# Performance work log

Hardware: AMD Instinct MI355X
Metric: run time of the kernel (lower is better)

The kernel has to match this reference:

```python
import jax, jax.numpy as jnp
import numpy as np

B, QLEN, PAST, D = 4, 2048, 2048, 2048


def setup_inputs() -> dict:
    key = jax.random.key(0)
    ks = jax.random.split(key, 6)
    x = jax.random.normal(ks[0], (B, QLEN, D), dtype=jnp.float32)
    past_k = jax.random.normal(ks[1], (B, PAST, D), dtype=jnp.float32)
    past_v = jax.random.normal(ks[2], (B, PAST, D), dtype=jnp.float32)
    # nn.Linear(model_dim, model_dim, bias=False) weights: [out, in]
    scale = 1.0 / np.sqrt(D)
    Wq = jax.random.uniform(ks[3], (D, D), dtype=jnp.float32, minval=-scale, maxval=scale)
    Wk = jax.random.uniform(ks[4], (D, D), dtype=jnp.float32, minval=-scale, maxval=scale)
    Wv = jax.random.uniform(ks[5], (D, D), dtype=jnp.float32, minval=-scale, maxval=scale)
    return {"x": x, "past_k": past_k, "past_v": past_v, "Wq": Wq, "Wk": Wk, "Wv": Wv}


def reference(x, past_k, past_v, Wq, Wk, Wv):
    # QKV projections (Linear: y = x @ W.T)
    q = jnp.einsum('btd,ed->bte', x, Wq)
    k = jnp.einsum('btd,ed->bte', x, Wk)
    v = jnp.einsum('btd,ed->bte', x, Wv)
    # KV cache update: concat along sequence dim (dim=1)
    full_k = jnp.concatenate([past_k, k], axis=1)  # [B, PAST+QLEN, D]
    full_v = jnp.concatenate([past_v, v], axis=1)
    # scaled dot-product attention, naive full score matrix as in source
    inv_sqrt_d = full_k.shape[-1] ** (-0.5)
    scores = jnp.einsum('bqd,bkd->bqk', q, full_k) * inv_sqrt_d  # [B, QLEN, PAST+QLEN]
    weights = jax.nn.softmax(scores, axis=-1)
    output = jnp.einsum('bqk,bkd->bqd', weights, full_v)
    return jnp.round(output, 4)
```

## Files before the change

kernel.cpp:

```cpp
#include <hip/hip_runtime.h>
#include <stdint.h>

#define QLEN  2048
#define PAST  2048
#define D_    2048
#define B_    4
#define LK    4096

typedef unsigned short ushort_t;
typedef __bf16  bf16x8 __attribute__((ext_vector_type(8)));
typedef float   f32x4  __attribute__((ext_vector_type(4)));

#define AS1 __attribute__((address_space(1)))
#define AS3 __attribute__((address_space(3)))

__device__ __forceinline__ ushort_t f2bf(float f) {
  union { float f; uint32_t u; } v; v.f = f;
  uint32_t u = v.u;
  u += 0x7FFFu + ((u >> 16) & 1u);
  return (ushort_t)(u >> 16);
}

__global__ __launch_bounds__(256) void diag_fill(float* __restrict__ out, int n4, float v0) {
  int i = blockIdx.x * 256 + threadIdx.x;
  if (i >= n4) return;
  float4 z = make_float4(0.f, 0.f, 0.f, 0.f);
  if (i == 0) z.x = v0;
  ((float4*)out)[i] = z;
}

__global__ __launch_bounds__(256) void cast_f32_bf16(const float* __restrict__ src,
                                                     ushort_t* __restrict__ dst, int n4) {
  int i = blockIdx.x * 256 + threadIdx.x;
  if (i >= n4) return;
  float4 v = ((const float4*)src)[i];
  ushort4 o; o.x = f2bf(v.x); o.y = f2bf(v.y); o.z = f2bf(v.z); o.w = f2bf(v.w);
  ((ushort4*)dst)[i] = o;
}

__global__ __launch_bounds__(256) void transpose_cast(const float* __restrict__ src0,
                                                      ushort_t* __restrict__ dst0,
                                                      size_t sbs, size_t dbs) {
  __shared__ float tile[64][65];
  const float* src = src0 + (size_t)blockIdx.z * sbs;
  ushort_t* dst = dst0 + (size_t)blockIdx.z * dbs;
  const int r0 = blockIdx.x * 64, c0 = blockIdx.y * 64;
  const int tid = threadIdx.x;
  const int rr = tid >> 4, cc = (tid & 15) * 4;
  #pragma unroll
  for (int it = 0; it < 4; ++it) {
    int r = rr + it * 16;
    float4 v = *(const float4*)(src + (size_t)(r0 + r) * D_ + c0 + cc);
    tile[r][cc] = v.x; tile[r][cc + 1] = v.y; tile[r][cc + 2] = v.z; tile[r][cc + 3] = v.w;
  }
  __syncthreads();
  const int cw = tid >> 4, rw = (tid & 15) * 4;
  #pragma unroll
  for (int it = 0; it < 4; ++it) {
    int c = cw + it * 16;
    ushort4 o;
    o.x = f2bf(tile[rw][c]);     o.y = f2bf(tile[rw + 1][c]);
    o.z = f2bf(tile[rw + 2][c]); o.w = f2bf(tile[rw + 3][c]);
    *(ushort4*)(dst + (size_t)(c0 + c) * PAST + r0 + rw) = o;
  }
}

struct GZ  { const ushort_t* A; const ushort_t* B0; const ushort_t* B1; void* C; };
struct GZV { GZ z[12]; };

template <bool OUT_BF16, bool SEG2>
__global__ __launch_bounds__(512, 2) void gemm_bt(GZV gz, int lda, int ldb, int K, int Kseg,
                                                  int ldc, float scale) {
  __shared__ ushort_t As[4][256 * 32];
  __shared__ ushort_t Bs[4][256 * 32];
  const GZ g = gz.z[blockIdx.z];

  const int tid  = threadIdx.x;
  const int lane = tid & 63;
  const int wave = tid >> 6;
  const int wm = wave >> 2, wn = wave & 3;
  const int m0 = blockIdx.y * 256, n0 = blockIdx.x * 256;

  const int r0s = tid >> 2;
  const int pgs = (tid & 3) ^ ((r0s >> 1) & 3);
  const ushort_t* gA  = g.A  + (size_t)(m0 + r0s) * lda + pgs * 8;
  const ushort_t* gB0 = g.B0 + (size_t)(n0 + r0s) * ldb + pgs * 8;
  const ushort_t* gB1 = SEG2 ? (g.B1 + (size_t)(n0 + r0s) * ldb + pgs * 8) : gB0;
  const size_t rstepA = (size_t)128 * lda;
  const size_t rstepB = (size_t)128 * ldb;
  const int ldsOff = tid * 8;

  const int laneRow = lane & 15, quad = lane >> 4;
  int offA[8], offB[4];
  #pragma unroll
  for (int mi = 0; mi < 8; ++mi) {
    const int row = wm * 128 + mi * 16 + laneRow;
    offA[mi] = row * 32 + ((quad ^ ((row >> 1) & 3)) * 8);
  }
  #pragma unroll
  for (int ni = 0; ni < 4; ++ni) {
    const int row = wn * 64 + ni * 16 + laneRow;
    offB[ni] = row * 32 + ((quad ^ ((row >> 1) & 3)) * 8);
  }

  const int NU = K >> 5;

  auto stageA = [&](int u) {
    const int k0 = u << 5;
    ushort_t* dst = &As[u & 3][0];
    __builtin_amdgcn_global_load_lds((const AS1 uint32_t*)(gA + k0),
                                     (AS3 uint32_t*)(dst + ldsOff), 16, 0, 0);
    __builtin_amdgcn_global_load_lds((const AS1 uint32_t*)(gA + rstepA + k0),
                                     (AS3 uint32_t*)(dst + 4096 + ldsOff), 16, 0, 0);
  };
  auto stageB = [&](int u) {
    const int k0 = u << 5;
    ushort_t* dst = &Bs[u & 3][0];
    const ushort_t* src = gB0;
    int kk = k0;
    if (SEG2 && k0 >= Kseg) { src = gB1; kk = k0 - Kseg; }
    __builtin_amdgcn_global_load_lds((const AS1 uint32_t*)(src + kk),
                                     (AS3 uint32_t*)(dst + ldsOff), 16, 0, 0);
    __builtin_amdgcn_global_load_lds((const AS1 uint32_t*)(src + rstepB + kk),
                                     (AS3 uint32_t*)(dst + 4096 + ldsOff), 16, 0, 0);
  };

  f32x4 acc[8][4] = {};

  stageA(0); stageB(0);
  stageA(1); stageB(1);
  stageA(2); stageB(2);
  __builtin_amdgcn_sched_barrier(0);
  asm volatile("s_waitcnt vmcnt(8)" ::: "memory");
  __builtin_amdgcn_s_barrier();
  __builtin_amdgcn_sched_barrier(0);

  for (int u = 0; u < NU; ++u) {
    const ushort_t* Au = &As[u & 3][0];
    const ushort_t* Bu = &Bs[u & 3][0];
    const bool pre = (u + 3) < NU;

    bf16x8 af[8], bf[4];
    #pragma unroll
    for (int mi = 0; mi < 8; ++mi) af[mi] = *(const bf16x8*)(Au + offA[mi]);
    #pragma unroll
    for (int ni = 0; ni < 4; ++ni) bf[ni] = *(const bf16x8*)(Bu + offB[ni]);

    if (pre) { stageA(u + 3); stageB(u + 3); }

    __builtin_amdgcn_s_setprio(1);
    #pragma unroll
    for (int mi = 0; mi < 8; ++mi)
      #pragma unroll
      for (int ni = 0; ni < 4; ++ni)
        acc[mi][ni] = __builtin_amdgcn_mfma_f32_16x16x32_bf16(af[mi], bf[ni], acc[mi][ni], 0, 0, 0);
    __builtin_amdgcn_s_setprio(0);

    __builtin_amdgcn_sched_barrier(0);
    if (pre) { asm volatile("s_waitcnt vmcnt(8)" ::: "memory"); }
    else     { asm volatile("s_waitcnt vmcnt(0)" ::: "memory"); }
    __builtin_amdgcn_s_barrier();
    __builtin_amdgcn_sched_barrier(0);
  }

  const int col = lane & 15;
  #pragma unroll
  for (int mi = 0; mi < 8; ++mi) {
    #pragma unroll
    for (int ni = 0; ni < 4; ++ni) {
      const int n = n0 + wn * 64 + ni * 16 + col;
      const int mb = m0 + wm * 128 + mi * 16 + quad * 4;
      #pragma unroll
      for (int r = 0; r < 4; ++r) {
        const int m = mb + r;
        const float v = acc[mi][ni][r] * scale;
        if constexpr (OUT_BF16)
          ((ushort_t*)g.C)[(size_t)m * ldc + n] = f2bf(v);
        else
          ((float*)g.C)[(size_t)m * ldc + n] = v;
      }
    }
  }
}

__global__ __launch_bounds__(256) void softmax_inplace(ushort_t* __restrict__ Sa,
                                                       ushort_t* __restrict__ Sb) {
  ushort_t* S = blockIdx.y ? Sb : Sa;
  const int row = blockIdx.x, tid = threadIdx.x;
  const int lane = tid & 63, wave = tid >> 6;
  ushort_t* s = S + (size_t)row * LK;

  float e[16];
  float m = -1e30f;
  #pragma unroll
  for (int i = 0; i < 2; ++i) {
    uint4 raw = *(const uint4*)(s + i * 2048 + tid * 8);
    const uint32_t u[4] = { raw.x, raw.y, raw.z, raw.w };
    #pragma unroll
    for (int j = 0; j < 4; ++j) {
      union { uint32_t u; float f; } lo, hi;
      lo.u = u[j] << 16;
      hi.u = u[j] & 0xFFFF0000u;
      e[i * 8 + j * 2] = lo.f;
      e[i * 8 + j * 2 + 1] = hi.f;
      m = fmaxf(m, fmaxf(lo.f, hi.f));
    }
  }
  #pragma unroll
  for (int off = 32; off > 0; off >>= 1) m = fmaxf(m, __shfl_xor(m, off));
  __shared__ float redm[4], reds[4];
  if (lane == 0) redm[wave] = m;
  __syncthreads();
  m = fmaxf(fmaxf(redm[0], redm[1]), fmaxf(redm[2], redm[3]));

  float sum = 0.f;
  #pragma unroll
  for (int i = 0; i < 16; ++i) { e[i] = __expf(e[i] - m); sum += e[i]; }
  #pragma unroll
  for (int off = 32; off > 0; off >>= 1) sum += __shfl_xor(sum, off);
  if (lane == 0) reds[wave] = sum;
  __syncthreads();
  sum = reds[0] + reds[1] + reds[2] + reds[3];
  const float inv = 1.0f / sum;

  #pragma unroll
  for (int i = 0; i < 2; ++i) {
    uint4 o;
    uint32_t* po = &o.x;
    #pragma unroll
    for (int j = 0; j < 4; ++j) {
      uint32_t lo = f2bf(e[i * 8 + j * 2] * inv);
      uint32_t hi = f2bf(e[i * 8 + j * 2 + 1] * inv);
      po[j] = lo | (hi << 16);
    }
    *(uint4*)(s + i * 2048 + tid * 8) = o;
  }
}

extern "C" void kernel_launch(void* const* d_in, const int* in_sizes, int n_in,
                              void* d_out, int out_size, void* d_ws, size_t ws_size,
                              hipStream_t stream) {
  const float* x      = (const float*)d_in[0];
  const float* past_k = (const float*)d_in[1];
  const float* past_v = (const float*)d_in[2];
  const float* Wq     = (const float*)d_in[3];
  const float* Wk     = (const float*)d_in[4];
  const float* Wv     = (const float*)d_in[5];
  float* out = (float*)d_out;

  const size_t MB = 1024 * 1024;
  const size_t NEED = 160 * MB;
  if (ws_size < NEED) {
    diag_fill<<<(out_size / 4 + 255) / 256, 256, 0, stream>>>(out, out_size / 4,
                                                              (float)((double)ws_size * 1e-9));
    return;
  }

  char* ws = (char*)d_ws;
  ushort_t* Qp[4]  = { (ushort_t*)(ws),            (ushort_t*)(ws + 8  * MB),
                       (ushort_t*)(ws + 32 * MB),  (ushort_t*)(ws + 40 * MB) };
  ushort_t* Knp[4] = { (ushort_t*)(ws + 16 * MB),  (ushort_t*)(ws + 24 * MB),
                       (ushort_t*)(ws + 48 * MB),  (ushort_t*)(ws + 56 * MB) };
  ushort_t* VTn = (ushort_t*)(ws + 64 * MB);
  ushort_t* xb  = (ushort_t*)(ws + 96 * MB);
  ushort_t* Wqb = (ushort_t*)(ws + 128 * MB);
  ushort_t* Wkb = (ushort_t*)(ws + 136 * MB);
  ushort_t* Wvb = (ushort_t*)(ws + 144 * MB);
  ushort_t* Kp  = (ushort_t*)(ws + 96 * MB);
  ushort_t* S0  = (ushort_t*)(ws + 128 * MB);
  ushort_t* S1  = (ushort_t*)(ws);
  ushort_t* VTp = (ushort_t*)(ws + 96 * MB);

  const size_t SLICE = (size_t)QLEN * D_;

  cast_f32_bf16<<<(B_ * SLICE / 4) / 256, 256, 0, stream>>>(x, xb, B_ * SLICE / 4);
  cast_f32_bf16<<<(D_ * D_ / 4) / 256, 256, 0, stream>>>(Wq, Wqb, D_ * D_ / 4);
  cast_f32_bf16<<<(D_ * D_ / 4) / 256, 256, 0, stream>>>(Wk, Wkb, D_ * D_ / 4);
  cast_f32_bf16<<<(D_ * D_ / 4) / 256, 256, 0, stream>>>(Wv, Wvb, D_ * D_ / 4);

  {
    GZV g{};
    for (int b = 0; b < B_; ++b) {
      const ushort_t* xbb = xb + (size_t)b * SLICE;
      g.z[b]     = { xbb, Wqb, Wqb, Qp[b] };
      g.z[4 + b] = { xbb, Wkb, Wkb, Knp[b] };
      g.z[8 + b] = { Wvb, xbb, xbb, VTn + (size_t)b * SLICE };
    }
    gemm_bt<true, false><<<dim3(8, 8, 12), 512, 0, stream>>>(g, D_, D_, D_, D_, D_, 1.0f);
  }

  cast_f32_bf16<<<(B_ * (size_t)PAST * D_ / 4) / 256, 256, 0, stream>>>(
      past_k, Kp, B_ * PAST * D_ / 4);

  const float sc = 0.022097086912079608f;

  {
    GZV g{};
    for (int j = 0; j < 2; ++j) {
      const int b = j;
      ushort_t* Sb = S0 + (size_t)j * QLEN * LK;
      g.z[2 * j]     = { Qp[b], Kp + (size_t)b * SLICE,  Kp + (size_t)b * SLICE,  Sb };
      g.z[2 * j + 1] = { Qp[b], Knp[b],                  Knp[b],                  Sb + PAST };
    }
    gemm_bt<true, false><<<dim3(8, 8, 4), 512, 0, stream>>>(g, D_, D_, D_, D_, LK, sc);
  }
  {
    GZV g{};
    for (int j = 0; j < 2; ++j) {
      const int b = 2 + j;
      ushort_t* Sb = S1 + (size_t)j * QLEN * LK;
      g.z[2 * j]     = { Qp[b], Kp + (size_t)b * SLICE,  Kp + (size_t)b * SLICE,  Sb };
      g.z[2 * j + 1] = { Qp[b], Knp[b],                  Knp[b],                  Sb + PAST };
    }
    gemm_bt<true, false><<<dim3(8, 8, 4), 512, 0, stream>>>(g, D_, D_, D_, D_, LK, sc);
  }

  transpose_cast<<<dim3(PAST / 64, D_ / 64, B_), 256, 0, stream>>>(
      past_v, VTp, (size_t)PAST * D_, (size_t)D_ * PAST);

  softmax_inplace<<<dim3(2 * QLEN, 2), 256, 0, stream>>>(S0, S1);

  {
    GZV g{};
    const ushort_t* Pb[4] = { S0, S0 + (size_t)QLEN * LK, S1, S1 + (size_t)QLEN * LK };
    for (int b = 0; b < B_; ++b)
      g.z[b] = { Pb[b], VTp + (size_t)b * SLICE, VTn + (size_t)b * SLICE,
                 out + (size_t)b * QLEN * D_ };
    gemm_bt<false, true><<<dim3(8, 8, 4), 512, 0, stream>>>(g, LK, PAST, LK, PAST, D_, 1.0f);
  }
}
```

Measured before the change: 704.2 us.

## Double-buffer LDS fragment reads across k-steps in the bf16 MFMA GEMM loop

Restructures the GEMM main loop, unrolled by two, so fragments for the next k-step are read from LDS while the current step's second half of MFMAs runs. Each step is split into two 4x4 MFMA groups, with register sets for A (rows 0-3 and 4-7) and two B buffers alternating between steps. The goal is to hide LDS read latency behind MFMA work. In exchange the global-to-LDS wait tightens from vmcnt(8) to vmcnt(4), which shrinks the effective global prefetch depth. It also raises register pressure and assumes an even number of k-steps.

```diff
diff --git a/kernel.cpp b/kernel.cpp
--- a/kernel.cpp
+++ b/kernel.cpp
@@ -131,36 +131,92 @@
   stageA(1); stageB(1);
   stageA(2); stageB(2);
   __builtin_amdgcn_sched_barrier(0);
-  asm volatile("s_waitcnt vmcnt(8)" ::: "memory");
+  asm volatile("s_waitcnt vmcnt(4)" ::: "memory");
   __builtin_amdgcn_s_barrier();
   __builtin_amdgcn_sched_barrier(0);
 
-  for (int u = 0; u < NU; ++u) {
-    const ushort_t* Au = &As[u & 3][0];
-    const ushort_t* Bu = &Bs[u & 3][0];
-    const bool pre = (u + 3) < NU;
-
-    bf16x8 af[8], bf[4];
-    #pragma unroll
-    for (int mi = 0; mi < 8; ++mi) af[mi] = *(const bf16x8*)(Au + offA[mi]);
-    #pragma unroll
-    for (int ni = 0; ni < 4; ++ni) bf[ni] = *(const bf16x8*)(Bu + offB[ni]);
-
-    if (pre) { stageA(u + 3); stageB(u + 3); }
-
-    __builtin_amdgcn_s_setprio(1);
-    #pragma unroll
-    for (int mi = 0; mi < 8; ++mi)
-      #pragma unroll
-      for (int ni = 0; ni < 4; ++ni)
-        acc[mi][ni] = __builtin_amdgcn_mfma_f32_16x16x32_bf16(af[mi], bf[ni], acc[mi][ni], 0, 0, 0);
-    __builtin_amdgcn_s_setprio(0);
-
-    __builtin_amdgcn_sched_barrier(0);
-    if (pre) { asm volatile("s_waitcnt vmcnt(8)" ::: "memory"); }
-    else     { asm volatile("s_waitcnt vmcnt(0)" ::: "memory"); }
-    __builtin_amdgcn_s_barrier();
-    __builtin_amdgcn_sched_barrier(0);
+  bf16x8 a03[4], a47[4], bA[4], bB[4];
+  #pragma unroll
+  for (int mi = 0; mi < 4; ++mi) a03[mi] = *(const bf16x8*)(&As[0][0] + offA[mi]);
+  #pragma unroll
+  for (int ni = 0; ni < 4; ++ni) bA[ni] = *(const bf16x8*)(&Bs[0][0] + offB[ni]);
+
+  for (int u = 0; u < NU; u += 2) {
+    {
+      const ushort_t* Au = &As[u & 3][0];
+      const ushort_t* An = &As[(u + 1) & 3][0];
+      const ushort_t* Bn = &Bs[(u + 1) & 3][0];
+      const bool pre = (u + 3) < NU;
+
+      #pragma unroll
+      for (int mi = 0; mi < 4; ++mi) a47[mi] = *(const bf16x8*)(Au + offA[4 + mi]);
+      if (pre) { stageA(u + 3); stageB(u + 3); }
+
+      __builtin_amdgcn_s_setprio(1);
+      #pragma unroll
+      for (int mi = 0; mi < 4; ++mi)
+        #pragma unroll
+        for (int ni = 0; ni < 4; ++ni)
+          acc[mi][ni] = __builtin_amdgcn_mfma_f32_16x16x32_bf16(a03[mi], bA[ni], acc[mi][ni], 0, 0, 0);
+      __builtin_amdgcn_s_setprio(0);
+
+      #pragma unroll
+      for (int mi = 0; mi < 4; ++mi) a03[mi] = *(const bf16x8*)(An + offA[mi]);
+      #pragma unroll
+      for (int ni = 0; ni < 4; ++ni) bB[ni] = *(const bf16x8*)(Bn + offB[ni]);
+
+      __builtin_amdgcn_s_setprio(1);
+      #pragma unroll
+      for (int mi = 0; mi < 4; ++mi)
+        #pragma unroll
+        for (int ni = 0; ni < 4; ++ni)
+          acc[4 + mi][ni] = __builtin_amdgcn_mfma_f32_16x16x32_bf16(a47[mi], bA[ni], acc[4 + mi][ni], 0, 0, 0);
+      __builtin_amdgcn_s_setprio(0);
+
+      __builtin_amdgcn_sched_barrier(0);
+      if (pre) { asm volatile("s_waitcnt vmcnt(4)" ::: "memory"); }
+      else     { asm volatile("s_waitcnt vmcnt(0)" ::: "memory"); }
+      __builtin_amdgcn_s_barrier();
+      __builtin_amdgcn_sched_barrier(0);
+    }
+    {
+      const int uo = u + 1;
+      const ushort_t* Au = &As[uo & 3][0];
+      const ushort_t* An = &As[(uo + 1) & 3][0];
+      const ushort_t* Bn = &Bs[(uo + 1) & 3][0];
+      const bool pre = (uo + 3) < NU;
+
+      #pragma unroll
+      for (int mi = 0; mi < 4; ++mi) a47[mi] = *(const bf16x8*)(Au + offA[4 + mi]);
+      if (pre) { stageA(uo + 3); stageB(uo + 3); }
+
+      __builtin_amdgcn_s_setprio(1);
+      #pragma unroll
+      for (int mi = 0; mi < 4; ++mi)
+        #pragma unroll
+        for (int ni = 0; ni < 4; ++ni)
+          acc[mi][ni] = __builtin_amdgcn_mfma_f32_16x16x32_bf16(a03[mi], bB[ni], acc[mi][ni], 0, 0, 0);
+      __builtin_amdgcn_s_setprio(0);
+
+      #pragma unroll
+      for (int mi = 0; mi < 4; ++mi) a03[mi] = *(const bf16x8*)(An + offA[mi]);
+      #pragma unroll
+      for (int ni = 0; ni < 4; ++ni) bA[ni] = *(const bf16x8*)(Bn + offB[ni]);
+
+      __builtin_amdgcn_s_setprio(1);
+      #pragma unroll
+      for (int mi = 0; mi < 4; ++mi)
+        #pragma unroll
+        for (int ni = 0; ni < 4; ++ni)
+          acc[4 + mi][ni] = __builtin_amdgcn_mfma_f32_16x16x32_bf16(a47[mi], bB[ni], acc[4 + mi][ni], 0, 0, 0);
+      __builtin_amdgcn_s_setprio(0);
+
+      __builtin_amdgcn_sched_barrier(0);
+      if (pre) { asm volatile("s_waitcnt vmcnt(4)" ::: "memory"); }
+      else     { asm volatile("s_waitcnt vmcnt(0)" ::: "memory"); }
+      __builtin_amdgcn_s_barrier();
+      __builtin_amdgcn_sched_barrier(0);
+    }
   }
 
   const int col = lane & 15;
```

Measured after the change: 755.8 us. 7.3% more time.
